# Kernel optimization log

Hardware: AMD Instinct MI355X
Metric: run time of the kernel (lower is better)

Reference implementation:

```python
import jax, jax.numpy as jnp
import numpy as np

EMB = 1024
HEADS = 16
HEAD_SIZE = EMB // HEADS


def setup_inputs() -> dict:
    key = jax.random.key(0)
    ks = jax.random.split(key, 10)
    B, L = 2, 2048
    s = 1.0 / np.sqrt(EMB)
    inp = {
        "x": jax.random.normal(ks[0], (B, L, EMB), jnp.float32),
        "ln_g": jnp.ones((EMB,), jnp.float32),
        "ln_b": jnp.zeros((EMB,), jnp.float32),
        "Wq": jax.random.normal(ks[1], (EMB, EMB), jnp.float32) * s,
        "bq": jnp.zeros((EMB,), jnp.float32),
        "Wk": jax.random.normal(ks[2], (EMB, EMB), jnp.float32) * s,
        "bk": jnp.zeros((EMB,), jnp.float32),
        "Wv": jax.random.normal(ks[3], (EMB, EMB), jnp.float32) * s,
        "bv": jnp.zeros((EMB,), jnp.float32),
        "Wo": jax.random.normal(ks[4], (EMB, EMB), jnp.float32) * s,
        "bo": jnp.zeros((EMB,), jnp.float32),
    }
    return inp


def _attn_block(x, ln_g, ln_b, Wq, bq, Wk, bk, Wv, bv, Wo, bo):
    B, L, D = x.shape
    # LayerNorm (eps=1e-5 as torch default)
    mu = jnp.mean(x, axis=-1, keepdims=True)
    var = jnp.mean(jnp.square(x - mu), axis=-1, keepdims=True)
    h = (x - mu) * jax.lax.rsqrt(var + 1e-5) * ln_g + ln_b
    # QKV projections (torch Linear: x @ W.T + b), split heads -> [B,H,L,hs]
    def heads(y):
        return y.reshape(B, L, HEADS, HEAD_SIZE).transpose(0, 2, 1, 3)
    q = heads(h @ Wq.T + bq)
    k = heads(h @ Wk.T + bk)
    v = heads(h @ Wv.T + bv)
    # scaled dot-product attention (no mask; dropout = identity in eval)
    scores = jnp.einsum("bhqd,bhkd->bhqk", q, k) * (HEAD_SIZE ** -0.5)
    w = jax.nn.softmax(scores, axis=-1)
    o = jnp.einsum("bhqk,bhkd->bhqd", w, v)
    o = o.transpose(0, 2, 1, 3).reshape(B, L, D)
    return o @ Wo.T + bo


def reference(x, ln_g, ln_b, Wq, bq, Wk, bk, Wv, bv, Wo, bo):
    return _attn_block(x, ln_g, ln_b, Wq, bq, Wk, bk, Wv, bv, Wo, bo)
```

## Files before the change

### kernel.cpp

```cpp
#include <hip/hip_runtime.h>
#include <stdint.h>

#define EMB 1024
#define SEQL 2048
#define HEADS 16
#define HS 64

typedef __attribute__((ext_vector_type(8))) short bfx8;
typedef __attribute__((ext_vector_type(4))) float f32x4;
typedef __attribute__((ext_vector_type(16))) float f32x16;
typedef __attribute__((ext_vector_type(4))) unsigned short us4;

__device__ __forceinline__ unsigned short f2bf(float f) {
  union { float f; unsigned u; } x; x.f = f;
  unsigned r = x.u + 0x7fffu + ((x.u >> 16) & 1u);
  return (unsigned short)(r >> 16);
}

__device__ __forceinline__ unsigned cvtpk(float lo, float hi) {
  unsigned r;
  asm("v_cvt_pk_bf16_f32 %0, %1, %2" : "=v"(r) : "v"(lo), "v"(hi));
  return r;
}

__device__ __forceinline__ float expv(float x) {
  float r;
  asm("v_exp_f32 %0, %1" : "=v"(r) : "v"(x));
  return r;
}

__device__ __forceinline__ float max3f(float a, float b, float c) {
  float r;
  asm("v_max3_f32 %0, %1, %2, %3" : "=v"(r) : "v"(a), "v"(b), "v"(c));
  return r;
}

__device__ __forceinline__ void gll16(const void* g, void* l) {
  __builtin_amdgcn_global_load_lds(
      (const __attribute__((address_space(1))) unsigned int*)g,
      (__attribute__((address_space(3))) unsigned int*)l, 16, 0, 0);
}

__global__ __launch_bounds__(256) void ln_kernel(
    const float* __restrict__ x, const float* __restrict__ gam,
    const float* __restrict__ bet, unsigned short* __restrict__ h) {
  const int row = blockIdx.x;
  const int tid = threadIdx.x;
  const float4 v = reinterpret_cast<const float4*>(x + (size_t)row * EMB)[tid];
  float s = v.x + v.y + v.z + v.w;
  float sq = v.x * v.x + v.y * v.y + v.z * v.z + v.w * v.w;
  #pragma unroll
  for (int m = 1; m < 64; m <<= 1) {
    s += __shfl_xor(s, m, 64);
    sq += __shfl_xor(sq, m, 64);
  }
  __shared__ float red[8];
  const int lane = tid & 63, wave = tid >> 6;
  if (lane == 0) { red[wave] = s; red[wave + 4] = sq; }
  __syncthreads();
  s = red[0] + red[1] + red[2] + red[3];
  sq = red[4] + red[5] + red[6] + red[7];
  const float mu = s * (1.0f / EMB);
  const float var = sq * (1.0f / EMB) - mu * mu;
  const float rs = rsqrtf(var + 1e-5f);
  const float4 gg = reinterpret_cast<const float4*>(gam)[tid];
  const float4 bb = reinterpret_cast<const float4*>(bet)[tid];
  us4 o;
  o.x = f2bf((v.x - mu) * rs * gg.x + bb.x);
  o.y = f2bf((v.y - mu) * rs * gg.y + bb.y);
  o.z = f2bf((v.z - mu) * rs * gg.z + bb.z);
  o.w = f2bf((v.w - mu) * rs * gg.w + bb.w);
  reinterpret_cast<us4*>(h + (size_t)row * EMB)[tid] = o;
}

__global__ __launch_bounds__(256) void cvt_kernel(
    const float* __restrict__ s0, const float* __restrict__ s1,
    const float* __restrict__ s2, const float* __restrict__ s3,
    unsigned short* __restrict__ d) {
  const int m = blockIdx.x >> 10;
  const int blk = blockIdx.x & 1023;
  const float* s = (m == 0) ? s0 : (m == 1) ? s1 : (m == 2) ? s2 : s3;
  unsigned short* dd = d + (size_t)m * EMB * EMB;
  const int idx = blk * 256 + threadIdx.x;
  const float4 v = reinterpret_cast<const float4*>(s)[idx];
  us4 o;
  o.x = f2bf(v.x); o.y = f2bf(v.y); o.z = f2bf(v.z); o.w = f2bf(v.w);
  reinterpret_cast<us4*>(dd)[idx] = o;
}

__device__ __forceinline__ void gemm_tile(
    const unsigned short* __restrict__ Ag, const unsigned short* __restrict__ Bg,
    int m0, int n0, int K, char* lA, char* lB, f32x4 acc[4][4]) {
  const int tid = threadIdx.x;
  const int lane = tid & 63, wave = tid >> 6;
  const int g = lane >> 4, c = lane & 15;
  const int wr = wave >> 1, wc = wave & 1;

  const f32x4 zero = {0.f, 0.f, 0.f, 0.f};
  #pragma unroll
  for (int i = 0; i < 4; ++i)
    #pragma unroll
    for (int j = 0; j < 4; ++j) acc[i][j] = zero;

  const int Dbase = (wave * 4 * 64 + lane) * 16;
  for (int k0 = 0; k0 < K; k0 += 64) {
    __syncthreads();
    #pragma unroll
    for (int i = 0; i < 4; ++i) {
      const int Db = Dbase + i * 1024;
      const int row = Db >> 7;
      const int col = ((Db & 127) ^ ((row & 7) << 4)) >> 1;
      gll16(Ag + (size_t)(m0 + row) * K + (k0 + col), lA + (wave * 4 + i) * 1024);
      gll16(Bg + (size_t)(n0 + row) * K + (k0 + col), lB + (wave * 4 + i) * 1024);
    }
    __syncthreads();
    #pragma unroll
    for (int kf = 0; kf < 2; ++kf) {
      bfx8 af[4], bfr[4];
      #pragma unroll
      for (int i = 0; i < 4; ++i) {
        const int ra = wr * 64 + i * 16 + c;
        af[i] = *(const bfx8*)(lA + ra * 128 + ((kf * 64 + g * 16) ^ ((ra & 7) << 4)));
        const int rb = wc * 64 + i * 16 + c;
        bfr[i] = *(const bfx8*)(lB + rb * 128 + ((kf * 64 + g * 16) ^ ((rb & 7) << 4)));
      }
      #pragma unroll
      for (int i = 0; i < 4; ++i)
        #pragma unroll
        for (int j = 0; j < 4; ++j)
          acc[i][j] = __builtin_amdgcn_mfma_f32_16x16x32_bf16(af[i], bfr[j], acc[i][j], 0, 0, 0);
    }
  }
}

__global__ __launch_bounds__(256, 2) void qkv_gemm(
    const unsigned short* __restrict__ h, const unsigned short* __restrict__ wbf,
    const float* __restrict__ bq, const float* __restrict__ bk,
    const float* __restrict__ bv, unsigned short* __restrict__ qb,
    unsigned short* __restrict__ kb, unsigned short* __restrict__ vtb) {
  __shared__ char lA[16384];
  __shared__ char lB[16384];
  f32x4 acc[4][4];
  const int m0 = blockIdx.x * 128;
  const int n0g = blockIdx.y * 128;
  const int mat = n0g >> 10;
  const int n0 = n0g & 1023;
  gemm_tile(h, wbf + (size_t)mat * EMB * EMB, m0, n0, EMB, lA, lB, acc);

  const float* bias = (mat == 0) ? bq : (mat == 1) ? bk : bv;
  const int lane = threadIdx.x & 63, wave = threadIdx.x >> 6;
  const int g = lane >> 4, c = lane & 15;
  const int wr = wave >> 1, wc = wave & 1;
  #pragma unroll
  for (int i = 0; i < 4; ++i) {
    #pragma unroll
    for (int j = 0; j < 4; ++j) {
      const int col = n0 + wc * 64 + j * 16 + c;
      const float bz = bias[col];
      const int hh = col >> 6, d = col & 63;
      #pragma unroll
      for (int r = 0; r < 4; ++r) {
        const int row = m0 + wr * 64 + i * 16 + 4 * g + r;
        const int bidx = row >> 11, l = row & 2047;
        const unsigned short bv16 = f2bf(acc[i][j][r] + bz);
        if (mat < 2) {
          unsigned short* dst = (mat == 0) ? qb : kb;
          dst[(((size_t)(bidx * HEADS + hh) * SEQL + l) << 6) + d] = bv16;
        } else {
          vtb[((size_t)(bidx * HEADS + hh) * HS + d) * SEQL + l] = bv16;
        }
      }
    }
  }
}

__global__ __launch_bounds__(256, 2) void attn_kernel(
    const unsigned short* __restrict__ qb, const unsigned short* __restrict__ kb,
    const unsigned short* __restrict__ vtb, unsigned short* __restrict__ ob) {
  __shared__ char lK[2][8192];
  __shared__ char lV[2][8192];
  const int tid = threadIdx.x, lane = tid & 63, wave = tid >> 6;
  const int l31 = lane & 31, hi = lane >> 5;
  const int sw = (l31 & 7) << 4;
  const int qblk = blockIdx.x;
  const int bh = blockIdx.y;
  const unsigned short* qp = qb + (size_t)bh * SEQL * HS;
  const unsigned short* kp = kb + (size_t)bh * SEQL * HS;
  const unsigned short* vp = vtb + (size_t)bh * HS * SEQL;
  const int qbase = qblk * 128 + wave * 32;

  bfx8 aq[4];
  #pragma unroll
  for (int kf = 0; kf < 4; ++kf)
    aq[kf] = *(const bfx8*)(qp + (size_t)(qbase + l31) * HS + kf * 16 + hi * 8);

  const float SCL = 0.125f * 1.44269504089f;
  const float THR = 11.5416f;
  const bfx8 vone = {0x3F80, 0x3F80, 0x3F80, 0x3F80, 0x3F80, 0x3F80, 0x3F80, 0x3F80};

  float mst = -INFINITY;
  f32x16 oacc0, oacc1, lacc;
  const f32x16 zero16 = {0.f,0.f,0.f,0.f,0.f,0.f,0.f,0.f,0.f,0.f,0.f,0.f,0.f,0.f,0.f,0.f};
  oacc0 = zero16; oacc1 = zero16; lacc = zero16;

  const int sbase = wave * 2048;
  const int Db0 = sbase + lane * 16, Db1 = Db0 + 1024;
  const int sr0 = Db0 >> 7, sr1 = Db1 >> 7;
  const int sc0 = ((Db0 & 127) ^ ((sr0 & 7) << 4)) >> 1;
  const int sc1 = ((Db1 & 127) ^ ((sr1 & 7) << 4)) >> 1;
  const unsigned short* k0s = kp + (size_t)sr0 * HS + sc0;
  const unsigned short* k1s = kp + (size_t)sr1 * HS + sc1;
  const unsigned short* v0s = vp + (size_t)sr0 * SEQL + sc0;
  const unsigned short* v1s = vp + (size_t)sr1 * SEQL + sc1;

  gll16(k0s, lK[0] + sbase); gll16(k1s, lK[0] + sbase + 1024);
  gll16(v0s, lV[0] + sbase); gll16(v1s, lV[0] + sbase + 1024);
  __syncthreads();

  const unsigned short* kf0 = k0s + 64 * HS;
  const unsigned short* kf1 = k1s + 64 * HS;
  const unsigned short* vf0 = v0s + 64;
  const unsigned short* vf1 = v1s + 64;

  auto step = [&](const char* lKc, const char* lVc, char* nK, char* nV, int t0) {
    if (t0 + 64 < SEQL) {
      gll16(kf0, nK + sbase); gll16(kf1, nK + sbase + 1024);
      gll16(vf0, nV + sbase); gll16(vf1, nV + sbase + 1024);
      kf0 += 64 * HS; kf1 += 64 * HS; vf0 += 64; vf1 += 64;
    }

    f32x16 sa = zero16, sb = zero16;
    __builtin_amdgcn_s_setprio(1);
    #pragma unroll
    for (int kf = 0; kf < 4; ++kf) {
      const int ko = (32 * kf + 16 * hi) ^ sw;
      const bfx8 a0 = *(const bfx8*)(lKc + l31 * 128 + ko);
      const bfx8 a1 = *(const bfx8*)(lKc + l31 * 128 + 4096 + ko);
      sa = __builtin_amdgcn_mfma_f32_32x32x16_bf16(a0, aq[kf], sa, 0, 0, 0);
      sb = __builtin_amdgcn_mfma_f32_32x32x16_bf16(a1, aq[kf], sb, 0, 0, 0);
    }
    __builtin_amdgcn_s_setprio(0);

    float m0 = max3f(sa[0], sa[1], sa[2]);
    float m1 = max3f(sa[3], sa[4], sa[5]);
    float m2 = max3f(sa[6], sa[7], sa[8]);
    float m3 = max3f(sa[9], sa[10], sa[11]);
    float m4 = max3f(sa[12], sa[13], sa[14]);
    float n0 = max3f(sb[0], sb[1], sb[2]);
    float n1 = max3f(sb[3], sb[4], sb[5]);
    float n2 = max3f(sb[6], sb[7], sb[8]);
    float n3 = max3f(sb[9], sb[10], sb[11]);
    float n4 = max3f(sb[12], sb[13], sb[14]);
    m0 = max3f(m0, m1, m2);
    m3 = max3f(m3, m4, sa[15]);
    n0 = max3f(n0, n1, n2);
    n3 = max3f(n3, n4, sb[15]);
    const float sm = fmaxf(fmaxf(m0, m3), fmaxf(n0, n3));

    if (__any(sm * SCL > mst + THR)) {
      float mt = sm * SCL;
      mt = fmaxf(mt, __shfl_xor(mt, 32, 64));
      const float mn = fmaxf(mst, mt);
      const float al = exp2f(mst - mn);
      mst = mn;
      #pragma unroll
      for (int r = 0; r < 16; ++r) {
        const int qi = (r & 3) + 8 * (r >> 2) + 4 * hi;
        const float alq = __shfl(al, qi, 64);
        lacc[r] *= alq;
        oacc0[r] *= alq;
        oacc1[r] *= alq;
      }
    }

    #pragma unroll
    for (int r = 0; r < 16; ++r) {
      sa[r] = expv(fmaf(sa[r], SCL, -mst));
      sb[r] = expv(fmaf(sb[r], SCL, -mst));
    }

    __builtin_amdgcn_s_setprio(1);
    #pragma unroll
    for (int kf = 0; kf < 4; ++kf) {
      const int bb = 8 * (kf & 1);
      float p0, p1, p2, p3, p4, p5, p6, p7;
      if (kf < 2) {
        p0 = sa[bb + 0]; p1 = sa[bb + 1]; p2 = sa[bb + 2]; p3 = sa[bb + 3];
        p4 = sa[bb + 4]; p5 = sa[bb + 5]; p6 = sa[bb + 6]; p7 = sa[bb + 7];
      } else {
        p0 = sb[bb + 0]; p1 = sb[bb + 1]; p2 = sb[bb + 2]; p3 = sb[bb + 3];
        p4 = sb[bb + 4]; p5 = sb[bb + 5]; p6 = sb[bb + 6]; p7 = sb[bb + 7];
      }
      unsigned w0 = cvtpk(p0, p1), w2 = cvtpk(p4, p5);
      unsigned w1 = cvtpk(p2, p3), w3 = cvtpk(p6, p7);
      asm("v_permlane32_swap_b32 %0, %1" : "+v"(w0), "+v"(w2));
      asm("v_permlane32_swap_b32 %0, %1" : "+v"(w1), "+v"(w3));
      union { unsigned u[4]; bfx8 v; } pa;
      pa.u[0] = w0; pa.u[1] = w1; pa.u[2] = w2; pa.u[3] = w3;
      lacc = __builtin_amdgcn_mfma_f32_32x32x16_bf16(pa.v, vone, lacc, 0, 0, 0);
      const int vo = (32 * kf + 16 * hi) ^ sw;
      const bfx8 b0 = *(const bfx8*)(lVc + l31 * 128 + vo);
      const bfx8 b1 = *(const bfx8*)(lVc + l31 * 128 + 4096 + vo);
      oacc0 = __builtin_amdgcn_mfma_f32_32x32x16_bf16(pa.v, b0, oacc0, 0, 0, 0);
      oacc1 = __builtin_amdgcn_mfma_f32_32x32x16_bf16(pa.v, b1, oacc1, 0, 0, 0);
    }
    __builtin_amdgcn_s_setprio(0);

    __syncthreads();
  };

  for (int t0 = 0; t0 < SEQL; t0 += 128) {
    step(lK[0], lV[0], lK[1], lV[1], t0);
    step(lK[1], lV[1], lK[0], lV[0], t0 + 64);
  }

  const int b = bh >> 4, hh = bh & 15;
  #pragma unroll
  for (int r = 0; r < 16; ++r) {
    const float inv = 1.f / lacc[r];
    const int row = qbase + (r & 3) + 8 * (r >> 2) + 4 * hi;
    unsigned short* orow = ob + (size_t)(b * SEQL + row) * EMB + hh * 64;
    orow[l31] = f2bf(oacc0[r] * inv);
    orow[32 + l31] = f2bf(oacc1[r] * inv);
  }
}

__global__ __launch_bounds__(256, 2) void out_gemm(
    const unsigned short* __restrict__ ob, const unsigned short* __restrict__ wo,
    const float* __restrict__ bo, float* __restrict__ out) {
  __shared__ char lA[16384];
  __shared__ char lB[16384];
  f32x4 acc[4][4];
  const int m0 = blockIdx.x * 128;
  const int n0 = blockIdx.y * 128;
  gemm_tile(ob, wo, m0, n0, EMB, lA, lB, acc);

  const int lane = threadIdx.x & 63, wave = threadIdx.x >> 6;
  const int g = lane >> 4, c = lane & 15;
  const int wr = wave >> 1, wc = wave & 1;
  #pragma unroll
  for (int i = 0; i < 4; ++i)
    #pragma unroll
    for (int j = 0; j < 4; ++j) {
      const int col = n0 + wc * 64 + j * 16 + c;
      const float bz = bo[col];
      #pragma unroll
      for (int r = 0; r < 4; ++r) {
        const int row = m0 + wr * 64 + i * 16 + 4 * g + r;
        out[(size_t)row * EMB + col] = acc[i][j][r] + bz;
      }
    }
}

extern "C" void kernel_launch(void* const* d_in, const int* in_sizes, int n_in,
                              void* d_out, int out_size, void* d_ws, size_t ws_size,
                              hipStream_t stream) {
  const float* x   = (const float*)d_in[0];
  const float* lng = (const float*)d_in[1];
  const float* lnb = (const float*)d_in[2];
  const float* Wq  = (const float*)d_in[3];
  const float* bq  = (const float*)d_in[4];
  const float* Wk  = (const float*)d_in[5];
  const float* bk  = (const float*)d_in[6];
  const float* Wv  = (const float*)d_in[7];
  const float* bv  = (const float*)d_in[8];
  const float* Wo  = (const float*)d_in[9];
  const float* bo  = (const float*)d_in[10];

  char* ws = (char*)d_ws;
  unsigned short* h   = (unsigned short*)(ws);
  unsigned short* wbf = (unsigned short*)(ws + 8388608);
  unsigned short* qb  = (unsigned short*)(ws + 16777216);
  unsigned short* kb  = (unsigned short*)(ws + 25165824);
  unsigned short* vtb = (unsigned short*)(ws + 33554432);
  unsigned short* ob  = (unsigned short*)(ws + 41943040);
  float* out = (float*)d_out;

  ln_kernel<<<dim3(4096), dim3(256), 0, stream>>>(x, lng, lnb, h);
  cvt_kernel<<<dim3(4096), dim3(256), 0, stream>>>(Wq, Wk, Wv, Wo, wbf);
  qkv_gemm<<<dim3(32, 24), dim3(256), 0, stream>>>(h, wbf, bq, bk, bv, qb, kb, vtb);
  attn_kernel<<<dim3(16, 32), dim3(256), 0, stream>>>(qb, kb, vtb, ob);
  out_gemm<<<dim3(32, 8), dim3(256), 0, stream>>>(ob, wbf + (size_t)3 * EMB * EMB, bo, out);
}
```

Before: 124.8 us.

## Split attention over two KV halves and merge partials in a combine kernel

Attention now runs with a third grid dimension that splits the key/value sequence in half, so twice as many blocks are launched. Each half writes unnormalized bf16 partial outputs plus per-row max and sum, and a new combine kernel rescales and merges them into the output buffer. The partial from the second half goes into the LayerNorm buffer, which is no longer needed by then. The change targets low occupancy on the attention grid, 512 blocks before. It costs an extra launch, extra memory traffic and an extra bf16 rounding of the partials, and launch bounds are also raised for the QKV and attention kernels.

Result: slower. 141.9 us (+13.7%).

```diff
diff --git a/kernel.cpp b/kernel.cpp
--- a/kernel.cpp
+++ b/kernel.cpp
@@ -133,7 +133,7 @@
   }
 }
 
-__global__ __launch_bounds__(256, 2) void qkv_gemm(
+__global__ __launch_bounds__(256, 3) void qkv_gemm(
     const unsigned short* __restrict__ h, const unsigned short* __restrict__ wbf,
     const float* __restrict__ bq, const float* __restrict__ bk,
     const float* __restrict__ bv, unsigned short* __restrict__ qb,
@@ -174,9 +174,10 @@
   }
 }
 
-__global__ __launch_bounds__(256, 2) void attn_kernel(
+__global__ __launch_bounds__(256, 4) void attn_kernel(
     const unsigned short* __restrict__ qb, const unsigned short* __restrict__ kb,
-    const unsigned short* __restrict__ vtb, unsigned short* __restrict__ ob) {
+    const unsigned short* __restrict__ vtb, unsigned short* __restrict__ p0,
+    unsigned short* __restrict__ p1, float* __restrict__ ml) {
   __shared__ char lK[2][8192];
   __shared__ char lV[2][8192];
   const int tid = threadIdx.x, lane = tid & 63, wave = tid >> 6;
@@ -184,9 +185,11 @@
   const int sw = (l31 & 7) << 4;
   const int qblk = blockIdx.x;
   const int bh = blockIdx.y;
+  const int kvh = blockIdx.z;
+  const int NK = SEQL / 2;
   const unsigned short* qp = qb + (size_t)bh * SEQL * HS;
-  const unsigned short* kp = kb + (size_t)bh * SEQL * HS;
-  const unsigned short* vp = vtb + (size_t)bh * HS * SEQL;
+  const unsigned short* kp = kb + (size_t)bh * SEQL * HS + (size_t)kvh * NK * HS;
+  const unsigned short* vp = vtb + (size_t)bh * HS * SEQL + (size_t)kvh * NK;
   const int qbase = qblk * 128 + wave * 32;
 
   bfx8 aq[4];
@@ -223,7 +226,7 @@
   const unsigned short* vf1 = v1s + 64;
 
   auto step = [&](const char* lKc, const char* lVc, char* nK, char* nV, int t0) {
-    if (t0 + 64 < SEQL) {
+    if (t0 + 64 < NK) {
       gll16(kf0, nK + sbase); gll16(kf1, nK + sbase + 1024);
       gll16(vf0, nV + sbase); gll16(vf1, nV + sbase + 1024);
       kf0 += 64 * HS; kf1 += 64 * HS; vf0 += 64; vf1 += 64;
@@ -309,20 +312,60 @@
     __syncthreads();
   };
 
-  for (int t0 = 0; t0 < SEQL; t0 += 128) {
+  for (int t0 = 0; t0 < NK; t0 += 128) {
     step(lK[0], lV[0], lK[1], lV[1], t0);
     step(lK[1], lV[1], lK[0], lV[0], t0 + 64);
   }
 
+  unsigned short* pout = kvh ? p1 : p0;
   const int b = bh >> 4, hh = bh & 15;
+  float mq[16];
+  #pragma unroll
+  for (int r = 0; r < 16; ++r)
+    mq[r] = __shfl(mst, (r & 3) + 8 * (r >> 2) + 4 * hi, 64);
   #pragma unroll
   for (int r = 0; r < 16; ++r) {
-    const float inv = 1.f / lacc[r];
     const int row = qbase + (r & 3) + 8 * (r >> 2) + 4 * hi;
-    unsigned short* orow = ob + (size_t)(b * SEQL + row) * EMB + hh * 64;
-    orow[l31] = f2bf(oacc0[r] * inv);
-    orow[32 + l31] = f2bf(oacc1[r] * inv);
-  }
+    unsigned short* orow = pout + (size_t)(b * SEQL + row) * EMB + hh * 64;
+    orow[l31] = f2bf(oacc0[r]);
+    orow[32 + l31] = f2bf(oacc1[r]);
+  }
+  if (l31 == 0) {
+    float* mlb = ml + ((size_t)(kvh * 32 + bh) * SEQL + qbase) * 2;
+    #pragma unroll
+    for (int r = 0; r < 16; ++r) {
+      const int qi = (r & 3) + 8 * (r >> 2) + 4 * hi;
+      mlb[qi * 2] = mq[r];
+      mlb[qi * 2 + 1] = lacc[r];
+    }
+  }
+}
+
+__global__ __launch_bounds__(256) void combine_kernel(
+    unsigned short* __restrict__ p0, const unsigned short* __restrict__ p1,
+    const float* __restrict__ ml) {
+  const int row = blockIdx.x;
+  const int tid = threadIdx.x;
+  const int b = row >> 11, lq = row & 2047;
+  const int hh = tid >> 4;
+  const int bh = b * HEADS + hh;
+  const float2 a = *reinterpret_cast<const float2*>(ml + ((size_t)bh * SEQL + lq) * 2);
+  const float2 c = *reinterpret_cast<const float2*>(ml + ((size_t)(32 + bh) * SEQL + lq) * 2);
+  const float M = fmaxf(a.x, c.x);
+  const float w0 = exp2f(a.x - M), w1 = exp2f(c.x - M);
+  const float inv = 1.f / (a.y * w0 + c.y * w1);
+  const float s0 = w0 * inv, s1 = w1 * inv;
+  const us4 o0 = reinterpret_cast<const us4*>(p0 + (size_t)row * EMB)[tid];
+  const us4 o1 = reinterpret_cast<const us4*>(p1 + (size_t)row * EMB)[tid];
+  us4 o;
+  #pragma unroll
+  for (int j = 0; j < 4; ++j) {
+    union { unsigned u; float f; } x0, x1;
+    x0.u = (unsigned)o0[j] << 16;
+    x1.u = (unsigned)o1[j] << 16;
+    o[j] = f2bf(x0.f * s0 + x1.f * s1);
+  }
+  reinterpret_cast<us4*>(p0 + (size_t)row * EMB)[tid] = o;
 }
 
 __global__ __launch_bounds__(256, 2) void out_gemm(
@@ -374,11 +417,13 @@
   unsigned short* kb  = (unsigned short*)(ws + 25165824);
   unsigned short* vtb = (unsigned short*)(ws + 33554432);
   unsigned short* ob  = (unsigned short*)(ws + 41943040);
+  float* ml = (float*)(ws + 50331648);
   float* out = (float*)d_out;
 
   ln_kernel<<<dim3(4096), dim3(256), 0, stream>>>(x, lng, lnb, h);
   cvt_kernel<<<dim3(4096), dim3(256), 0, stream>>>(Wq, Wk, Wv, Wo, wbf);
   qkv_gemm<<<dim3(32, 24), dim3(256), 0, stream>>>(h, wbf, bq, bk, bv, qb, kb, vtb);
-  attn_kernel<<<dim3(16, 32), dim3(256), 0, stream>>>(qb, kb, vtb, ob);
+  attn_kernel<<<dim3(16, 32, 2), dim3(256), 0, stream>>>(qb, kb, vtb, ob, h, ml);
+  combine_kernel<<<dim3(4096), dim3(256), 0, stream>>>(ob, h, ml);
   out_gemm<<<dim3(32, 8), dim3(256), 0, stream>>>(ob, wbf + (size_t)3 * EMB * EMB, bo, out);
 }
```

## Deepen attention K/V prefetch to four LDS stages with vmcnt waits

Applied to the files above, without the earlier changes.

The attention kernel's K/V LDS ring grows from two to four buffers and now prefetches two tiles ahead. The per-step __syncthreads is replaced by explicit s_waitcnt vmcnt counts plus s_barrier, so loads for later tiles stay in flight while the current tile is computed. LDS use per block doubles to 64 KB, which may limit blocks per CU. The qkv_gemm launch bound is also raised to 3 blocks per CU, which constrains its register budget.

Result: no change. 123.9 us (-0.7%).

```diff
diff --git a/kernel.cpp b/kernel.cpp
--- a/kernel.cpp
+++ b/kernel.cpp
@@ -133,7 +133,7 @@
   }
 }
 
-__global__ __launch_bounds__(256, 2) void qkv_gemm(
+__global__ __launch_bounds__(256, 3) void qkv_gemm(
     const unsigned short* __restrict__ h, const unsigned short* __restrict__ wbf,
     const float* __restrict__ bq, const float* __restrict__ bk,
     const float* __restrict__ bv, unsigned short* __restrict__ qb,
@@ -177,8 +177,8 @@
 __global__ __launch_bounds__(256, 2) void attn_kernel(
     const unsigned short* __restrict__ qb, const unsigned short* __restrict__ kb,
     const unsigned short* __restrict__ vtb, unsigned short* __restrict__ ob) {
-  __shared__ char lK[2][8192];
-  __shared__ char lV[2][8192];
+  __shared__ char lK[4][8192];
+  __shared__ char lV[4][8192];
   const int tid = threadIdx.x, lane = tid & 63, wave = tid >> 6;
   const int l31 = lane & 31, hi = lane >> 5;
   const int sw = (l31 & 7) << 4;
@@ -215,19 +215,26 @@
 
   gll16(k0s, lK[0] + sbase); gll16(k1s, lK[0] + sbase + 1024);
   gll16(v0s, lV[0] + sbase); gll16(v1s, lV[0] + sbase + 1024);
-  __syncthreads();
-
-  const unsigned short* kf0 = k0s + 64 * HS;
-  const unsigned short* kf1 = k1s + 64 * HS;
-  const unsigned short* vf0 = v0s + 64;
-  const unsigned short* vf1 = v1s + 64;
-
-  auto step = [&](const char* lKc, const char* lVc, char* nK, char* nV, int t0) {
-    if (t0 + 64 < SEQL) {
+  gll16(k0s + 64 * HS, lK[1] + sbase); gll16(k1s + 64 * HS, lK[1] + sbase + 1024);
+  gll16(v0s + 64, lV[1] + sbase); gll16(v1s + 64, lV[1] + sbase + 1024);
+
+  const unsigned short* kf0 = k0s + 2 * 64 * HS;
+  const unsigned short* kf1 = k1s + 2 * 64 * HS;
+  const unsigned short* vf0 = v0s + 2 * 64;
+  const unsigned short* vf1 = v1s + 2 * 64;
+
+  auto step = [&](const char* lKc, const char* lVc, char* nK, char* nV,
+                  const int wait, const bool doStage) {
+    if (doStage) {
       gll16(kf0, nK + sbase); gll16(kf1, nK + sbase + 1024);
       gll16(vf0, nV + sbase); gll16(vf1, nV + sbase + 1024);
       kf0 += 64 * HS; kf1 += 64 * HS; vf0 += 64; vf1 += 64;
     }
+    if (wait == 8)      asm volatile("s_waitcnt vmcnt(8)" ::: "memory");
+    else if (wait == 4) asm volatile("s_waitcnt vmcnt(4)" ::: "memory");
+    else                asm volatile("s_waitcnt vmcnt(0)" ::: "memory");
+    __builtin_amdgcn_s_barrier();
+    __builtin_amdgcn_sched_barrier(0);
 
     f32x16 sa = zero16, sb = zero16;
     __builtin_amdgcn_s_setprio(1);
@@ -305,14 +312,18 @@
       oacc1 = __builtin_amdgcn_mfma_f32_32x32x16_bf16(pa.v, b1, oacc1, 0, 0, 0);
     }
     __builtin_amdgcn_s_setprio(0);
-
-    __syncthreads();
   };
 
-  for (int t0 = 0; t0 < SEQL; t0 += 128) {
-    step(lK[0], lV[0], lK[1], lV[1], t0);
-    step(lK[1], lV[1], lK[0], lV[0], t0 + 64);
-  }
+  for (int t = 0; t < 28; t += 4) {
+    step(lK[0], lV[0], lK[2], lV[2], 8, true);
+    step(lK[1], lV[1], lK[3], lV[3], 8, true);
+    step(lK[2], lV[2], lK[0], lV[0], 8, true);
+    step(lK[3], lV[3], lK[1], lV[1], 8, true);
+  }
+  step(lK[0], lV[0], lK[2], lV[2], 8, true);
+  step(lK[1], lV[1], lK[3], lV[3], 8, true);
+  step(lK[2], lV[2], lK[0], lV[0], 4, false);
+  step(lK[3], lV[3], lK[1], lV[1], 0, false);
 
   const int b = bh >> 4, hh = bh & 15;
   #pragma unroll
```
